# Kernel tuning notes

Measured on AMD Instinct MI355X. Metric: run time of the kernel, lower is better.

The kernel has to match this reference:

```python
import jax, jax.numpy as jnp
import numpy as np

B, T, I, H = 128, 2048, 64, 128


def setup_inputs() -> dict:
    key = jax.random.key(0)
    ks = jax.random.split(key, 7)
    return {
        "input_data": jax.random.normal(ks[0], (B, T, I), dtype=jnp.float32),
        "h0": jax.random.normal(ks[1], (B, H), dtype=jnp.float32),
        "c0": jax.random.normal(ks[2], (B, H), dtype=jnp.float32),
        "W_ih": jax.random.normal(ks[3], (4 * H, I), dtype=jnp.float32) * 0.05,
        "W_hh": jax.random.normal(ks[4], (4 * H, H), dtype=jnp.float32) * 0.05,
        "b_ih": jax.random.normal(ks[5], (4 * H,), dtype=jnp.float32) * 0.05,
        "b_hh": jax.random.normal(ks[6], (4 * H,), dtype=jnp.float32) * 0.05,
    }


def reference(input_data, h0, c0, W_ih, W_hh, b_ih, b_hh):
    # Precompute input projections for all timesteps: [B, T, 4H]
    x_proj = jnp.einsum('bti,gi->btg', input_data, W_ih) + b_ih + b_hh

    def step(carry, xg):
        h, c = carry                      # [B, H]
        gates = xg + h @ W_hh.T           # [B, 4H]
        i_g, f_g, g_g, o_g = jnp.split(gates, 4, axis=-1)  # PyTorch order i,f,g,o
        i_g = jax.nn.sigmoid(i_g)
        f_g = jax.nn.sigmoid(f_g)
        g_g = jnp.tanh(g_g)
        o_g = jax.nn.sigmoid(o_g)
        c_new = f_g * c + i_g * g_g
        h_new = o_g * jnp.tanh(c_new)
        return (h_new, c_new), h_new

    (h_last, c_last), hs = jax.lax.scan(step, (h0, c0), jnp.swapaxes(x_proj, 0, 1))
    input_encoded = jnp.swapaxes(hs, 0, 1)  # [B, T, H]
    return (h_last[None], input_encoded)
```

## Files before the change

kernel.cpp:

```cpp
#include <hip/hip_runtime.h>

#define BB 128
#define TT 2048
#define II 64
#define HH 128
#define GG 512

typedef _Float16 h2 __attribute__((ext_vector_type(2)));

__device__ __forceinline__ h2 mkh2(float a, float b) {
    h2 r; r.x = (_Float16)a; r.y = (_Float16)b; return r;
}

__device__ __forceinline__ h2 u2h(unsigned u) {
    return __builtin_bit_cast(h2, u);
}

__device__ __forceinline__ float fdot2f(h2 a, h2 b, float c) {
#if __has_builtin(__builtin_amdgcn_fdot2)
    return __builtin_amdgcn_fdot2(a, b, c, false);
#else
    return fmaf((float)a.y, (float)b.y, fmaf((float)a.x, (float)b.x, c));
#endif
}

__device__ __forceinline__ float rcp_fast(float x) {
    return __builtin_amdgcn_rcpf(x);
}

__device__ __forceinline__ float tanh_fast(float x) {
    return fmaf(rcp_fast(1.0f + __expf(-2.0f * x)), 2.0f, -1.0f);
}

template <int CTRL>
__device__ __forceinline__ float dppq(float x) {
#if __has_builtin(__builtin_amdgcn_update_dpp)
    int i = __builtin_bit_cast(int, x);
    int r = __builtin_amdgcn_update_dpp(i, i, CTRL, 0xF, 0xF, true);
    return __builtin_bit_cast(float, r);
#else
    return __shfl_xor(x, (CTRL == 177) ? 1 : (CTRL == 78) ? 2 : 3, 4);
#endif
}

__global__ __launch_bounds__(512, 2) void lstm_fused_kernel(
    const float* __restrict__ input,
    const float* __restrict__ h0,
    const float* __restrict__ c0,
    const float* __restrict__ W_ih,
    const float* __restrict__ W_hh,
    const float* __restrict__ b_ih,
    const float* __restrict__ b_hh,
    float* __restrict__ out)
{
    __shared__ __align__(16) h2 s_x[2][II / 2];
    __shared__ __align__(16) h2 s_h[2][HH / 2];

    const int tid  = threadIdx.x;
    const int b    = blockIdx.x;
    const int lane = tid & 63;
    const int w    = tid >> 6;
    const int gt   = lane & 3;
    const int j    = (w << 4) | (lane >> 2);
    const int row  = (gt << 7) | j;

    h2 wih[II / 2];
    h2 whh[HH / 2];
    {
        const float4* p = reinterpret_cast<const float4*>(W_ih + row * II);
#pragma unroll
        for (int q = 0; q < II / 4; ++q) {
            float4 v = p[q];
            wih[2 * q]     = mkh2(v.x, v.y);
            wih[2 * q + 1] = mkh2(v.z, v.w);
        }
    }
    {
        const float4* p = reinterpret_cast<const float4*>(W_hh + row * HH);
#pragma unroll
        for (int q = 0; q < HH / 4; ++q) {
            float4 v = p[q];
            whh[2 * q]     = mkh2(v.x, v.y);
            whh[2 * q + 1] = mkh2(v.z, v.w);
        }
    }
    const float bias = b_ih[row] + b_hh[row];

    float c = c0[(size_t)b * HH + j];
    if (tid < 64) {
        float2 hv = reinterpret_cast<const float2*>(h0 + (size_t)b * HH)[tid];
        s_h[0][tid] = mkh2(hv.x, hv.y);
    }

    const float2* xin = reinterpret_cast<const float2*>(input) + (size_t)b * TT * 32 + tid;
    float2 xb0, xb1, xb2, xb3;
    if (tid < 32) {
        xb0 = xin[(size_t)0 * 32];
        xb1 = xin[(size_t)1 * 32];
        xb2 = xin[(size_t)2 * 32];
        xb3 = xin[(size_t)3 * 32];
        s_x[0][tid] = mkh2(xb0.x, xb0.y);
        xb0 = xin[(size_t)4 * 32];
    }
    __syncthreads();

    float* out_h = out;
    float* out_e = out + BB * HH;
    float hlast = 0.0f;

    auto step = [&](int t, float2& xbn) {
        const int cb = t & 1, nb = cb ^ 1;

        if (tid < 32) {
            s_x[nb][tid] = mkh2(xbn.x, xbn.y);
            int tn = t + 5; if (tn > TT - 1) tn = TT - 1;
            xbn = xin[(size_t)tn * 32];
        }

        const uint4* sx4 = reinterpret_cast<const uint4*>(s_x[cb]);
        const uint4* sh4 = reinterpret_cast<const uint4*>(s_h[cb]);
        float a0 = bias, a1 = 0.0f, a2 = 0.0f, a3 = 0.0f;
#pragma unroll
        for (int q = 0; q < 8; ++q) {
            uint4 v = sx4[q];
            a0 = fdot2f(wih[4 * q + 0], u2h(v.x), a0);
            a1 = fdot2f(wih[4 * q + 1], u2h(v.y), a1);
            a2 = fdot2f(wih[4 * q + 2], u2h(v.z), a2);
            a3 = fdot2f(wih[4 * q + 3], u2h(v.w), a3);
        }
#pragma unroll
        for (int q = 0; q < 16; ++q) {
            uint4 v = sh4[q];
            a0 = fdot2f(whh[4 * q + 0], u2h(v.x), a0);
            a1 = fdot2f(whh[4 * q + 1], u2h(v.y), a1);
            a2 = fdot2f(whh[4 * q + 2], u2h(v.z), a2);
            a3 = fdot2f(whh[4 * q + 3], u2h(v.w), a3);
        }
        float gate = (a0 + a1) + (a2 + a3);

        float pre = (gt == 2) ? 2.0f * gate : gate;
        float sg  = rcp_fast(1.0f + __expf(-pre));
        float act = (gt == 2) ? fmaf(sg, 2.0f, -1.0f) : sg;

        float v0 = act;
        float v1 = dppq<177>(act);
        float v2 = dppq<78>(act);
        float v3 = dppq<27>(act);
        float sA = (gt & 1) ? v1 : v0;
        float sB = (gt & 1) ? v3 : v2;
        float sC = (gt & 1) ? v0 : v1;
        float sD = (gt & 1) ? v2 : v3;
        float iv = (gt & 2) ? sB : sA;
        float gv = (gt & 2) ? sA : sB;
        float fv = (gt & 2) ? sD : sC;
        float ov = (gt & 2) ? sC : sD;

        c = fmaf(fv, c, iv * gv);
        float hv = ov * tanh_fast(c);
        hlast = hv;

        if (gt == 0) reinterpret_cast<_Float16*>(s_h[nb])[j] = (_Float16)hv;
        if (gt == 1) out_e[((size_t)b * TT + t) * HH + j] = hv;

        __syncthreads();
    };

    for (int t0 = 0; t0 < TT; t0 += 4) {
        step(t0 + 0, xb1);
        step(t0 + 1, xb2);
        step(t0 + 2, xb3);
        step(t0 + 3, xb0);
    }

    if (gt == 2) out_h[(size_t)b * HH + j] = hlast;
}

extern "C" void kernel_launch(void* const* d_in, const int* in_sizes, int n_in,
                              void* d_out, int out_size, void* d_ws, size_t ws_size,
                              hipStream_t stream) {
    const float* input = (const float*)d_in[0];
    const float* h0    = (const float*)d_in[1];
    const float* c0    = (const float*)d_in[2];
    const float* W_ih  = (const float*)d_in[3];
    const float* W_hh  = (const float*)d_in[4];
    const float* b_ih  = (const float*)d_in[5];
    const float* b_hh  = (const float*)d_in[6];
    float* out = (float*)d_out;

    hipLaunchKernelGGL(lstm_fused_kernel, dim3(BB), dim3(GG), 0, stream,
                       input, h0, c0, W_ih, W_hh, b_ih, b_hh, out);
}
```

Measured before the change: 1.608 ms.

## Halve block size with two hidden units per thread and readlane broadcasts

Each thread now computes gate rows for two hidden units, so the block shrinks from 512 to 256 threads (4 waves), which lowers per-step barrier cost. The x and h vectors share one LDS buffer. Each lane reads one word from it, and the operands are broadcast with v_readlane instead of every lane reading the whole vector from LDS. The aim is to cut LDS traffic and sync overhead on the serial recurrence. The cost is twice the weight registers per thread, lower occupancy, and 96 scalar readlanes per step that may serialize.

Measured after the change: 2.534 ms. 1.58x slower.

```diff
diff --git a/kernel.cpp b/kernel.cpp
--- a/kernel.cpp
+++ b/kernel.cpp
@@ -4,7 +4,6 @@
 #define TT 2048
 #define II 64
 #define HH 128
-#define GG 512
 
 typedef _Float16 h2 __attribute__((ext_vector_type(2)));
 
@@ -14,6 +13,10 @@
 
 __device__ __forceinline__ h2 u2h(unsigned u) {
     return __builtin_bit_cast(h2, u);
+}
+
+__device__ __forceinline__ unsigned h2u(h2 v) {
+    return __builtin_bit_cast(unsigned, v);
 }
 
 __device__ __forceinline__ float fdot2f(h2 a, h2 b, float c) {
@@ -30,6 +33,10 @@
 
 __device__ __forceinline__ float tanh_fast(float x) {
     return fmaf(rcp_fast(1.0f + __expf(-2.0f * x)), 2.0f, -1.0f);
+}
+
+__device__ __forceinline__ h2 bcast(unsigned v, int q) {
+    return u2h((unsigned)__builtin_amdgcn_readlane((int)v, q));
 }
 
 template <int CTRL>
@@ -43,7 +50,7 @@
 #endif
 }
 
-__global__ __launch_bounds__(512, 2) void lstm_fused_kernel(
+__global__ __launch_bounds__(256, 1) void lstm_fused_kernel(
     const float* __restrict__ input,
     const float* __restrict__ h0,
     const float* __restrict__ c0,
@@ -53,43 +60,49 @@
     const float* __restrict__ b_hh,
     float* __restrict__ out)
 {
-    __shared__ __align__(16) h2 s_x[2][II / 2];
-    __shared__ __align__(16) h2 s_h[2][HH / 2];
+    __shared__ __align__(16) unsigned s_z[2][96];
 
     const int tid  = threadIdx.x;
     const int b    = blockIdx.x;
+    const int w    = tid >> 6;
     const int lane = tid & 63;
-    const int w    = tid >> 6;
     const int gt   = lane & 3;
-    const int j    = (w << 4) | (lane >> 2);
-    const int row  = (gt << 7) | j;
-
-    h2 wih[II / 2];
-    h2 whh[HH / 2];
+    const int k    = lane >> 2;
+    const int j1   = (w << 4) | k;
+    const int j2   = j1 + 64;
+    const int row1 = (gt << 7) | j1;
+    const int row2 = (gt << 7) | j2;
+
+    h2 wx1[II / 2], wx2[II / 2];
+    h2 wh1[HH / 2], wh2[HH / 2];
     {
-        const float4* p = reinterpret_cast<const float4*>(W_ih + row * II);
+        const float4* p1 = reinterpret_cast<const float4*>(W_ih + row1 * II);
+        const float4* p2 = reinterpret_cast<const float4*>(W_ih + row2 * II);
 #pragma unroll
         for (int q = 0; q < II / 4; ++q) {
-            float4 v = p[q];
-            wih[2 * q]     = mkh2(v.x, v.y);
-            wih[2 * q + 1] = mkh2(v.z, v.w);
+            float4 a = p1[q], c = p2[q];
+            wx1[2 * q] = mkh2(a.x, a.y); wx1[2 * q + 1] = mkh2(a.z, a.w);
+            wx2[2 * q] = mkh2(c.x, c.y); wx2[2 * q + 1] = mkh2(c.z, c.w);
         }
     }
     {
-        const float4* p = reinterpret_cast<const float4*>(W_hh + row * HH);
+        const float4* p1 = reinterpret_cast<const float4*>(W_hh + row1 * HH);
+        const float4* p2 = reinterpret_cast<const float4*>(W_hh + row2 * HH);
 #pragma unroll
         for (int q = 0; q < HH / 4; ++q) {
-            float4 v = p[q];
-            whh[2 * q]     = mkh2(v.x, v.y);
-            whh[2 * q + 1] = mkh2(v.z, v.w);
-        }
-    }
-    const float bias = b_ih[row] + b_hh[row];
-
-    float c = c0[(size_t)b * HH + j];
+            float4 a = p1[q], c = p2[q];
+            wh1[2 * q] = mkh2(a.x, a.y); wh1[2 * q + 1] = mkh2(a.z, a.w);
+            wh2[2 * q] = mkh2(c.x, c.y); wh2[2 * q + 1] = mkh2(c.z, c.w);
+        }
+    }
+    const float bias1 = b_ih[row1] + b_hh[row1];
+    const float bias2 = b_ih[row2] + b_hh[row2];
+
+    float c1 = c0[(size_t)b * HH + j1];
+    float c2 = c0[(size_t)b * HH + j2];
     if (tid < 64) {
         float2 hv = reinterpret_cast<const float2*>(h0 + (size_t)b * HH)[tid];
-        s_h[0][tid] = mkh2(hv.x, hv.y);
+        s_z[0][32 + tid] = h2u(mkh2(hv.x, hv.y));
     }
 
     const float2* xin = reinterpret_cast<const float2*>(input) + (size_t)b * TT * 32 + tid;
@@ -99,68 +112,99 @@
         xb1 = xin[(size_t)1 * 32];
         xb2 = xin[(size_t)2 * 32];
         xb3 = xin[(size_t)3 * 32];
-        s_x[0][tid] = mkh2(xb0.x, xb0.y);
+        s_z[0][tid] = h2u(mkh2(xb0.x, xb0.y));
         xb0 = xin[(size_t)4 * 32];
     }
     __syncthreads();
 
     float* out_h = out;
     float* out_e = out + BB * HH;
-    float hlast = 0.0f;
+    float hl1 = 0.0f, hl2 = 0.0f;
 
     auto step = [&](int t, float2& xbn) {
         const int cb = t & 1, nb = cb ^ 1;
 
         if (tid < 32) {
-            s_x[nb][tid] = mkh2(xbn.x, xbn.y);
+            s_z[nb][tid] = h2u(mkh2(xbn.x, xbn.y));
             int tn = t + 5; if (tn > TT - 1) tn = TT - 1;
             xbn = xin[(size_t)tn * 32];
         }
 
-        const uint4* sx4 = reinterpret_cast<const uint4*>(s_x[cb]);
-        const uint4* sh4 = reinterpret_cast<const uint4*>(s_h[cb]);
-        float a0 = bias, a1 = 0.0f, a2 = 0.0f, a3 = 0.0f;
-#pragma unroll
-        for (int q = 0; q < 8; ++q) {
-            uint4 v = sx4[q];
-            a0 = fdot2f(wih[4 * q + 0], u2h(v.x), a0);
-            a1 = fdot2f(wih[4 * q + 1], u2h(v.y), a1);
-            a2 = fdot2f(wih[4 * q + 2], u2h(v.z), a2);
-            a3 = fdot2f(wih[4 * q + 3], u2h(v.w), a3);
-        }
-#pragma unroll
-        for (int q = 0; q < 16; ++q) {
-            uint4 v = sh4[q];
-            a0 = fdot2f(whh[4 * q + 0], u2h(v.x), a0);
-            a1 = fdot2f(whh[4 * q + 1], u2h(v.y), a1);
-            a2 = fdot2f(whh[4 * q + 2], u2h(v.z), a2);
-            a3 = fdot2f(whh[4 * q + 3], u2h(v.w), a3);
-        }
-        float gate = (a0 + a1) + (a2 + a3);
-
-        float pre = (gt == 2) ? 2.0f * gate : gate;
-        float sg  = rcp_fast(1.0f + __expf(-pre));
-        float act = (gt == 2) ? fmaf(sg, 2.0f, -1.0f) : sg;
-
-        float v0 = act;
-        float v1 = dppq<177>(act);
-        float v2 = dppq<78>(act);
-        float v3 = dppq<27>(act);
-        float sA = (gt & 1) ? v1 : v0;
-        float sB = (gt & 1) ? v3 : v2;
-        float sC = (gt & 1) ? v0 : v1;
-        float sD = (gt & 1) ? v2 : v3;
-        float iv = (gt & 2) ? sB : sA;
-        float gv = (gt & 2) ? sA : sB;
-        float fv = (gt & 2) ? sD : sC;
-        float ov = (gt & 2) ? sC : sD;
-
-        c = fmaf(fv, c, iv * gv);
-        float hv = ov * tanh_fast(c);
-        hlast = hv;
-
-        if (gt == 0) reinterpret_cast<_Float16*>(s_h[nb])[j] = (_Float16)hv;
-        if (gt == 1) out_e[((size_t)b * TT + t) * HH + j] = hv;
+        unsigned v0 = s_z[cb][lane];
+        unsigned v1 = s_z[cb][64 + (lane & 31)];
+
+        float a10 = bias1, a11 = 0.f, a12 = 0.f, a13 = 0.f;
+        float a20 = bias2, a21 = 0.f, a22 = 0.f, a23 = 0.f;
+
+#pragma unroll
+        for (int q = 0; q < 32; ++q) {
+            h2 z = bcast(v0, q);
+            switch (q & 3) {
+                case 0: a10 = fdot2f(wx1[q], z, a10); a20 = fdot2f(wx2[q], z, a20); break;
+                case 1: a11 = fdot2f(wx1[q], z, a11); a21 = fdot2f(wx2[q], z, a21); break;
+                case 2: a12 = fdot2f(wx1[q], z, a12); a22 = fdot2f(wx2[q], z, a22); break;
+                default: a13 = fdot2f(wx1[q], z, a13); a23 = fdot2f(wx2[q], z, a23); break;
+            }
+        }
+#pragma unroll
+        for (int p = 0; p < 32; ++p) {
+            h2 z = bcast(v0, 32 + p);
+            switch (p & 3) {
+                case 0: a10 = fdot2f(wh1[p], z, a10); a20 = fdot2f(wh2[p], z, a20); break;
+                case 1: a11 = fdot2f(wh1[p], z, a11); a21 = fdot2f(wh2[p], z, a21); break;
+                case 2: a12 = fdot2f(wh1[p], z, a12); a22 = fdot2f(wh2[p], z, a22); break;
+                default: a13 = fdot2f(wh1[p], z, a13); a23 = fdot2f(wh2[p], z, a23); break;
+            }
+        }
+#pragma unroll
+        for (int p = 32; p < 64; ++p) {
+            h2 z = bcast(v1, p - 32);
+            switch (p & 3) {
+                case 0: a10 = fdot2f(wh1[p], z, a10); a20 = fdot2f(wh2[p], z, a20); break;
+                case 1: a11 = fdot2f(wh1[p], z, a11); a21 = fdot2f(wh2[p], z, a21); break;
+                case 2: a12 = fdot2f(wh1[p], z, a12); a22 = fdot2f(wh2[p], z, a22); break;
+                default: a13 = fdot2f(wh1[p], z, a13); a23 = fdot2f(wh2[p], z, a23); break;
+            }
+        }
+        float g1 = (a10 + a11) + (a12 + a13);
+        float g2 = (a20 + a21) + (a22 + a23);
+
+        float p1 = (gt == 2) ? 2.0f * g1 : g1;
+        float p2 = (gt == 2) ? 2.0f * g2 : g2;
+        float s1 = rcp_fast(1.0f + __expf(-p1));
+        float s2 = rcp_fast(1.0f + __expf(-p2));
+        float act1 = (gt == 2) ? fmaf(s1, 2.0f, -1.0f) : s1;
+        float act2 = (gt == 2) ? fmaf(s2, 2.0f, -1.0f) : s2;
+
+        float x1a = dppq<177>(act1), x1b = dppq<78>(act1), x1c = dppq<27>(act1);
+        float x2a = dppq<177>(act2), x2b = dppq<78>(act2), x2c = dppq<27>(act2);
+
+        auto gates = [&](float v0_, float v1_, float v2_, float v3_,
+                         float& iv, float& fv, float& gv, float& ov) {
+            float sA = (gt & 1) ? v1_ : v0_;
+            float sB = (gt & 1) ? v3_ : v2_;
+            float sC = (gt & 1) ? v0_ : v1_;
+            float sD = (gt & 1) ? v2_ : v3_;
+            iv = (gt & 2) ? sB : sA;
+            gv = (gt & 2) ? sA : sB;
+            fv = (gt & 2) ? sD : sC;
+            ov = (gt & 2) ? sC : sD;
+        };
+        float iv1, fv1, gv1, ov1, iv2, fv2, gv2, ov2;
+        gates(act1, x1a, x1b, x1c, iv1, fv1, gv1, ov1);
+        gates(act2, x2a, x2b, x2c, iv2, fv2, gv2, ov2);
+
+        c1 = fmaf(fv1, c1, iv1 * gv1);
+        c2 = fmaf(fv2, c2, iv2 * gv2);
+        float hv1 = ov1 * tanh_fast(c1);
+        float hv2 = ov2 * tanh_fast(c2);
+        hl1 = hv1; hl2 = hv2;
+
+        _Float16* zh = reinterpret_cast<_Float16*>(&s_z[nb][32]);
+        if (gt == 0) zh[j1] = (_Float16)hv1;
+        if (gt == 1) zh[j2] = (_Float16)hv2;
+        if (gt == 2) out_e[((size_t)b * TT + t) * HH + j1] = hv1;
+        if (gt == 3) out_e[((size_t)b * TT + t) * HH + j2] = hv2;
 
         __syncthreads();
     };
@@ -172,7 +216,8 @@
         step(t0 + 3, xb0);
     }
 
-    if (gt == 2) out_h[(size_t)b * HH + j] = hlast;
+    if (gt == 0) out_h[(size_t)b * HH + j1] = hl1;
+    if (gt == 1) out_h[(size_t)b * HH + j2] = hl2;
 }
 
 extern "C" void kernel_launch(void* const* d_in, const int* in_sizes, int n_in,
@@ -187,6 +232,6 @@
     const float* b_hh  = (const float*)d_in[6];
     float* out = (float*)d_out;
 
-    hipLaunchKernelGGL(lstm_fused_kernel, dim3(BB), dim3(GG), 0, stream,
+    hipLaunchKernelGGL(lstm_fused_kernel, dim3(BB), dim3(256), 0, stream,
                        input, h0, c0, W_ih, W_hh, b_ih, b_hh, out);
 }
```
